# Performance work log

Hardware: AMD Instinct MI355X
Metric: run time of the kernel (lower is better)

The kernel has to match this reference:

```python
import jax, jax.numpy as jnp
import numpy as np

B, T, FB, C = 2, 256, 128, 128
H_T, H_F, BAND = 4, 4, 16
INNER = 4 * C


def setup_inputs() -> dict:
    key = jax.random.key(0)
    ks = jax.random.split(key, 8)
    g = lambda k, shp: jax.random.normal(k, shp, jnp.float32) * 0.02
    return {
        "x": jax.random.normal(ks[0], (B, T, FB, C), jnp.float32),
        # temporal pre-norm + MHA (in_proj [3C,C], out_proj [C,C])
        "ln_t_w": jnp.ones((C,), jnp.float32), "ln_t_b": jnp.zeros((C,), jnp.float32),
        "t_wi": g(ks[1], (3 * C, C)), "t_bi": jnp.zeros((3 * C,), jnp.float32),
        "t_wo": g(ks[2], (C, C)), "t_bo": jnp.zeros((C,), jnp.float32),
        # frequency pre-norm + MHA
        "ln_f_w": jnp.ones((C,), jnp.float32), "ln_f_b": jnp.zeros((C,), jnp.float32),
        "f_wi": g(ks[3], (3 * C, C)), "f_bi": jnp.zeros((3 * C,), jnp.float32),
        "f_wo": g(ks[4], (C, C)), "f_bo": jnp.zeros((C,), jnp.float32),
        # FFN pre-norm + two linears
        "ln_n_w": jnp.ones((C,), jnp.float32), "ln_n_b": jnp.zeros((C,), jnp.float32),
        "w1": g(ks[5], (INNER, C)), "b1": jnp.zeros((INNER,), jnp.float32),
        "w2": g(ks[6], (C, INNER)), "b2": jnp.zeros((C,), jnp.float32),
    }


def _ln(x, w, b, eps=1e-5):
    mu = x.mean(-1, keepdims=True)
    var = ((x - mu) ** 2).mean(-1, keepdims=True)
    return (x - mu) * jax.lax.rsqrt(var + eps) * w + b


def _mha(x, wi, bi, wo, bo, h, mask):
    """torch.nn.MultiheadAttention equivalent. x: [..., S, C], mask: additive [S, S]."""
    c = x.shape[-1]
    dh = c // h
    qkv = x @ wi.T + bi
    q, k, v = jnp.split(qkv, 3, axis=-1)
    split = lambda t: t.reshape(t.shape[:-1] + (h, dh)).swapaxes(-2, -3)  # [..., h, S, dh]
    q, k, v = split(q), split(k), split(v)
    scores = jnp.einsum('...hqd,...hkd->...hqk', q, k) * (1.0 / np.sqrt(dh)) + mask
    attn = jax.nn.softmax(scores, axis=-1)
    o = jnp.einsum('...hqk,...hkd->...hqd', attn, v)
    o = o.swapaxes(-2, -3).reshape(x.shape)
    return o @ wo.T + bo


def _causal_mask(n):
    i = jnp.arange(n)
    return jnp.where(i[:, None] >= i[None, :], 0.0, -jnp.inf).astype(jnp.float32)


def _band_mask(n, band):
    i = jnp.arange(n)
    return jnp.where(jnp.abs(i[:, None] - i[None, :]) <= band, 0.0, -jnp.inf).astype(jnp.float32)


def reference(x, ln_t_w, ln_t_b, t_wi, t_bi, t_wo, t_bo,
              ln_f_w, ln_f_b, f_wi, f_bi, f_wo, f_bo,
              ln_n_w, ln_n_b, w1, b1, w2, b2):
    cm = _causal_mask(x.shape[1])      # [T, T]
    bm = _band_mask(x.shape[2], BAND)  # [F, F]
    # temporal causal MHSA per frequency bin (pre-norm residual)
    xt = _ln(x, ln_t_w, ln_t_b).transpose(0, 2, 1, 3)  # [B, F, T, C]
    x = x + _mha(xt, t_wi, t_bi, t_wo, t_bo, H_T, cm).transpose(0, 2, 1, 3)
    # banded local MHSA over frequency per time step
    xf = _ln(x, ln_f_w, ln_f_b)  # [B, T, F, C]
    x = x + _mha(xf, f_wi, f_bi, f_wo, f_bo, H_F, bm)
    # FFN (Linear -> exact GELU -> Linear)
    xn = _ln(x, ln_n_w, ln_n_b)
    h = jax.nn.gelu(xn @ w1.T + b1, approximate=False)
    x = x + (h @ w2.T + b2)
    return x
```

## Files before the change

kernel.cpp:

```cpp
#include <hip/hip_runtime.h>
#include <math.h>

typedef __bf16 bf16;
typedef __bf16 bf16x8 __attribute__((ext_vector_type(8)));
typedef __bf16 bf16x4 __attribute__((ext_vector_type(4)));
typedef __bf16 bf16x2 __attribute__((ext_vector_type(2)));
typedef float f32x4 __attribute__((ext_vector_type(4)));
typedef float f32x2 __attribute__((ext_vector_type(2)));
typedef float f32x16 __attribute__((ext_vector_type(16)));
typedef unsigned int u32;
typedef unsigned int u32x4 __attribute__((ext_vector_type(4)));

#define AS1 __attribute__((address_space(1)))
#define AS3 __attribute__((address_space(3)))

static __device__ __forceinline__ f32x4 mfma16(bf16x8 a, bf16x8 b, f32x4 c) {
    return __builtin_amdgcn_mfma_f32_16x16x32_bf16(a, b, c, 0, 0, 0);
}
static __device__ __forceinline__ f32x16 mfma32(bf16x8 a, bf16x8 b, f32x16 c) {
    return __builtin_amdgcn_mfma_f32_32x32x16_bf16(a, b, c, 0, 0, 0);
}
static __device__ __forceinline__ u32 pk2(float a, float b) {
    bf16x2 v; v[0] = (bf16)a; v[1] = (bf16)b;
    return __builtin_bit_cast(u32, v);
}
static __device__ __forceinline__ float gelu_f(float x) {
    float u = 0.7978845608f * x * __builtin_fmaf(0.044715f, x * x, 1.0f);
    float e = __expf(2.0f * u);
    return x - x * __builtin_amdgcn_rcpf(e + 1.0f);
}

__global__ __launch_bounds__(256) void cvt_w6(
    const float* __restrict__ s0, const float* __restrict__ s1,
    const float* __restrict__ s2, const float* __restrict__ s3,
    const float* __restrict__ s4, const float* __restrict__ s5,
    bf16* __restrict__ dst)
{
    int i = (blockIdx.x * 256 + threadIdx.x) * 4;
    const float* src; int off;
    if      (i <  49152) { src = s0; off = 0; }
    else if (i <  65536) { src = s1; off = 49152; }
    else if (i < 114688) { src = s2; off = 65536; }
    else if (i < 131072) { src = s3; off = 114688; }
    else if (i < 196608) { src = s4; off = 131072; }
    else                 { src = s5; off = 196608; }
    f32x4 v = *(const f32x4*)&src[i - off];
    bf16x4 b;
    b[0] = (bf16)v[0]; b[1] = (bf16)v[1]; b[2] = (bf16)v[2]; b[3] = (bf16)v[3];
    *(bf16x4*)&dst[i] = b;
}

template<int OUT_BF16, int RES, int RESBF, int GELU_, int LNA, int RMAP, int KT, int NT>
__global__ __launch_bounds__(256) void gemm_rw(
    const bf16* __restrict__ A, const bf16* __restrict__ W,
    const float* __restrict__ bias, const void* __restrict__ res,
    void* __restrict__ outp,
    const float* __restrict__ xf, const float* __restrict__ lnaw,
    const float* __restrict__ lnab)
{
    constexpr int N = NT * 128;
    __shared__ __align__(16) bf16 Bs[128 * 64];
    const int tid  = threadIdx.x;
    const int lane = tid & 63;
    const int w    = tid >> 6;
    const int li = lane & 15, g = lane >> 4;
    const int m0 = blockIdx.x * 64;
    const int arow = m0 + w * 16 + li;
    int srow = arow;
    if constexpr (RMAP) {
        int b = arow >> 15, t = (arow >> 7) & 255, f = arow & 127;
        srow = (b << 15) + (f << 8) + t;
    }
    const bf16* ap = A + (size_t)srow * KT;

    bf16x8 afrag[4];
    if constexpr (LNA) {
        int b = arow >> 15, f = (arow >> 8) & 127, t = arow & 255;
        const float* xp = xf + (((size_t)b * 256 + t) * 128 + f) * 128;
        f32x4 cv[8];
        #pragma unroll
        for (int cc = 0; cc < 4; ++cc) {
            cv[2 * cc]     = *(const f32x4*)&xp[cc * 32 + g * 8];
            cv[2 * cc + 1] = *(const f32x4*)&xp[cc * 32 + g * 8 + 4];
        }
        float sm = 0.f, sq = 0.f;
        #pragma unroll
        for (int i = 0; i < 8; ++i)
            #pragma unroll
            for (int j = 0; j < 4; ++j) { float v = cv[i][j]; sm += v; sq += v * v; }
        sm += __shfl_xor(sm, 16); sm += __shfl_xor(sm, 32);
        sq += __shfl_xor(sq, 16); sq += __shfl_xor(sq, 32);
        float mu = sm * 0.0078125f;
        float rs = rsqrtf(sq * 0.0078125f - mu * mu + 1e-5f);
        #pragma unroll
        for (int cc = 0; cc < 4; ++cc) {
            f32x4 w0 = *(const f32x4*)&lnaw[cc * 32 + g * 8];
            f32x4 w1 = *(const f32x4*)&lnaw[cc * 32 + g * 8 + 4];
            f32x4 b0 = *(const f32x4*)&lnab[cc * 32 + g * 8];
            f32x4 b1 = *(const f32x4*)&lnab[cc * 32 + g * 8 + 4];
            #pragma unroll
            for (int j = 0; j < 4; ++j) {
                afrag[cc][j]     = (bf16)((cv[2 * cc][j]     - mu) * rs * w0[j] + b0[j]);
                afrag[cc][4 + j] = (bf16)((cv[2 * cc + 1][j] - mu) * rs * w1[j] + b1[j]);
            }
        }
    } else if constexpr (KT == 128) {
        #pragma unroll
        for (int cc = 0; cc < 4; ++cc)
            afrag[cc] = *(const bf16x8*)&ap[cc * 32 + g * 8];
    }

    #pragma unroll
    for (int t = 0; t < NT; ++t) {
        const int n0 = t * 128;
        f32x4 acc[8] = {};

        #pragma unroll
        for (int k0 = 0; k0 < KT; k0 += 64) {
            #pragma unroll
            for (int it = 0; it < 4; ++it) {
                int idx = it * 256 + tid;
                int brow = idx >> 3, bch = idx & 7;
                const bf16* gp = W + (size_t)(n0 + brow) * KT + k0 + ((bch ^ (brow & 7)) * 8);
                __builtin_amdgcn_global_load_lds((AS1 void*)gp, (AS3 void*)(Bs + idx * 8), 16, 0, 0);
            }
            bf16x8 av0, av1;
            if constexpr (KT != 128) {
                av0 = *(const bf16x8*)&ap[k0 + g * 8];
                av1 = *(const bf16x8*)&ap[k0 + 32 + g * 8];
            }
            __syncthreads();
            #pragma unroll
            for (int kk = 0; kk < 2; ++kk) {
                bf16x8 av;
                if constexpr (KT == 128) av = afrag[(k0 >> 5) + kk];
                else                     av = kk ? av1 : av0;
                #pragma unroll
                for (int j = 0; j < 8; ++j) {
                    int brow = j * 16 + li;
                    int bch = (kk * 4 + g) ^ (li & 7);
                    bf16x8 bv = *(const bf16x8*)&Bs[brow * 64 + bch * 8];
                    acc[j] = mfma16(av, bv, acc[j]);
                }
            }
            __syncthreads();
        }

        float bcol[8];
        #pragma unroll
        for (int j = 0; j < 8; ++j) bcol[j] = bias[n0 + j * 16 + li];

        const int row0 = m0 + w * 16 + g * 4;
        #pragma unroll
        for (int r = 0; r < 4; ++r) {
            int row = row0 + r;
            #pragma unroll
            for (int j = 0; j < 8; ++j) {
                size_t off = (size_t)row * N + n0 + j * 16 + li;
                float v = acc[j][r] + bcol[j];
                if constexpr (RES) {
                    if constexpr (RESBF) v += (float)((const bf16*)res)[off];
                    else                 v += ((const float*)res)[off];
                }
                if constexpr (GELU_) v = gelu_f(v);
                if constexpr (OUT_BF16) ((bf16*)outp)[off] = (bf16)v;
                else                    ((float*)outp)[off] = v;
            }
        }
    }
}

__global__ __launch_bounds__(256) void ffn_fused(
    const bf16* __restrict__ A, const bf16* __restrict__ W1,
    const float* __restrict__ b1, const bf16* __restrict__ W2,
    const float* __restrict__ b2, const bf16* __restrict__ res,
    float* __restrict__ outp)
{
    __shared__ __align__(16) bf16 Bs[128 * 64];
    __shared__ __align__(16) bf16 hbuf[64 * 136];
    const int tid  = threadIdx.x;
    const int lane = tid & 63;
    const int w    = tid >> 6;
    const int li = lane & 15, g = lane >> 4;
    const int m0 = blockIdx.x * 64;
    const int arow = m0 + w * 16 + li;
    const bf16* ap = A + (size_t)arow * 128;

    bf16x8 axn[4];
    #pragma unroll
    for (int cc = 0; cc < 4; ++cc)
        axn[cc] = *(const bf16x8*)&ap[cc * 32 + g * 8];

    const int sidx_brow = tid >> 1;

    f32x4 oacc[8] = {};

    #pragma unroll
    for (int t = 0; t < 4; ++t) {
        f32x4 hacc[8] = {};
        #pragma unroll
        for (int k0 = 0; k0 < 128; k0 += 64) {
            #pragma unroll
            for (int it = 0; it < 4; ++it) {
                int idx = it * 256 + tid;
                int brow = idx >> 3, bch = idx & 7;
                const bf16* gp = W1 + (size_t)(t * 128 + brow) * 128 + k0 + ((bch ^ (brow & 7)) * 8);
                __builtin_amdgcn_global_load_lds((AS1 void*)gp, (AS3 void*)(Bs + idx * 8), 16, 0, 0);
            }
            __syncthreads();
            #pragma unroll
            for (int kk = 0; kk < 2; ++kk) {
                bf16x8 av = axn[(k0 >> 5) + kk];
                #pragma unroll
                for (int j = 0; j < 8; ++j) {
                    int brow = j * 16 + li;
                    int bch = (kk * 4 + g) ^ (li & 7);
                    bf16x8 bv = *(const bf16x8*)&Bs[brow * 64 + bch * 8];
                    hacc[j] = mfma16(av, bv, hacc[j]);
                }
            }
            __syncthreads();
        }

        #pragma unroll
        for (int it = 0; it < 4; ++it) {
            int idx = it * 256 + tid;
            int brow = idx >> 3, bch = idx & 7;
            const bf16* gp = W2 + (size_t)brow * 512 + t * 128 + ((bch ^ (brow & 7)) * 8);
            __builtin_amdgcn_global_load_lds((AS1 void*)gp, (AS3 void*)(Bs + idx * 8), 16, 0, 0);
        }

        float b1c[8];
        #pragma unroll
        for (int j = 0; j < 8; ++j) b1c[j] = b1[t * 128 + j * 16 + li];
        #pragma unroll
        for (int r = 0; r < 4; ++r) {
            int lrow = w * 16 + g * 4 + r;
            #pragma unroll
            for (int j = 0; j < 8; ++j)
                hbuf[lrow * 136 + j * 16 + li] = (bf16)gelu_f(hacc[j][r] + b1c[j]);
        }
        __syncthreads();

        bf16x8 ah[4];
        #pragma unroll
        for (int cc = 0; cc < 4; ++cc)
            ah[cc] = *(const bf16x8*)&hbuf[(w * 16 + li) * 136 + cc * 32 + g * 8];

        #pragma unroll
        for (int k0 = 0; k0 < 128; k0 += 64) {
            if (k0) {
                #pragma unroll
                for (int it = 0; it < 4; ++it) {
                    int idx = it * 256 + tid;
                    int brow = idx >> 3, bch = idx & 7;
                    const bf16* gp = W2 + (size_t)brow * 512 + t * 128 + k0 + ((bch ^ (brow & 7)) * 8);
                    __builtin_amdgcn_global_load_lds((AS1 void*)gp, (AS3 void*)(Bs + idx * 8), 16, 0, 0);
                }
                __syncthreads();
            }
            #pragma unroll
            for (int kk = 0; kk < 2; ++kk) {
                bf16x8 av = ah[(k0 >> 5) + kk];
                #pragma unroll
                for (int j = 0; j < 8; ++j) {
                    int brow = j * 16 + li;
                    int bch = (kk * 4 + g) ^ (li & 7);
                    bf16x8 bv = *(const bf16x8*)&Bs[brow * 64 + bch * 8];
                    oacc[j] = mfma16(av, bv, oacc[j]);
                }
            }
            __syncthreads();
        }
    }

    float b2c[8];
    #pragma unroll
    for (int j = 0; j < 8; ++j) b2c[j] = b2[j * 16 + li];
    const int row0 = m0 + w * 16 + g * 4;
    #pragma unroll
    for (int r = 0; r < 4; ++r) {
        int row = row0 + r;
        #pragma unroll
        for (int j = 0; j < 8; ++j) {
            size_t off = (size_t)row * 128 + j * 16 + li;
            float v = oacc[j][r] + b2c[j] + (float)res[off];
            outp[off] = v;
        }
    }
}

template<int MODE, int RESBF>
__global__ __launch_bounds__(256) void attn_fused(
    const bf16* __restrict__ qkv, const bf16* __restrict__ Wo,
    const float* __restrict__ bo, const void* __restrict__ res,
    bf16* __restrict__ xc, bf16* __restrict__ xn,
    const float* __restrict__ lnw, const float* __restrict__ lnb)
{
    constexpr int S = (MODE == 0) ? 256 : 128;
    __shared__ __align__(16) char smem[2 * 20480 + 2048];
    float* red = (float*)(smem + 40960);
    const int tid = threadIdx.x;
    const int lane = tid & 63;
    const int w = tid >> 6;
    const int hi = lane >> 5;
    const int q31 = lane & 31;
    const int s = blockIdx.x;
    const int qb = blockIdx.y * 64;

    const size_t base = (size_t)s * S * 384;
    const bf16* qp = qkv + base + w * 32;

    const float sc = 0.17677669529663687f;
    bf16x8 qA0, qA1, qB0, qB1;
    {
        bf16x8 r0 = *(const bf16x8*)&qp[(size_t)(qb + q31) * 384 + hi * 8];
        bf16x8 r1 = *(const bf16x8*)&qp[(size_t)(qb + q31) * 384 + 16 + hi * 8];
        bf16x8 r2 = *(const bf16x8*)&qp[(size_t)(qb + 32 + q31) * 384 + hi * 8];
        bf16x8 r3 = *(const bf16x8*)&qp[(size_t)(qb + 32 + q31) * 384 + 16 + hi * 8];
        #pragma unroll
        for (int e = 0; e < 8; ++e) {
            qA0[e] = (bf16)((float)r0[e] * sc);
            qA1[e] = (bf16)((float)r1[e] * sc);
            qB0[e] = (bf16)((float)r2[e] * sc);
            qB1[e] = (bf16)((float)r3[e] * sc);
        }
    }

    f32x16 OA = {}, OB = {};
    float lA = 0.f, lB = 0.f;

    int klo, khi;
    if constexpr (MODE == 0) { klo = 0; khi = qb + 64; }
    else {
        klo = (qb > 16 ? (qb - 16) : 0) & ~31;
        khi = (qb + 80 < S) ? (qb + 80) : S;
    }

    const int seg = tid & 15, rw = tid >> 4;
    const char* qc = (const char*)qkv + base * 2;
    const int wdst = (seg >> 2) * 2560 + rw * 80 + (seg & 3) * 16;

    u32x4 rk0, rk1, rv0, rv1;
    auto gload = [&](int k0) {
        const char* r0 = qc + (size_t)(k0 + rw) * 768;
        const char* r1 = qc + (size_t)(k0 + rw + 16) * 768;
        rk0 = *(const u32x4*)(r0 + 256 + seg * 16);
        rk1 = *(const u32x4*)(r1 + 256 + seg * 16);
        rv0 = *(const u32x4*)(r0 + 512 + seg * 16);
        rv1 = *(const u32x4*)(r1 + 512 + seg * 16);
    };
    auto swrite = [&](char* buf) {
        *(u32x4*)(buf + wdst)                = rk0;
        *(u32x4*)(buf + wdst + 1280)         = rk1;
        *(u32x4*)(buf + 10240 + wdst)        = rv0;
        *(u32x4*)(buf + 10240 + wdst + 1280) = rv1;
    };

    gload(klo);
    swrite(smem);
    __syncthreads();
    int cur = 0;

    for (int k0 = klo; k0 < khi; k0 += 32) {
        bool notlast = (k0 + 32 < khi);
        if (notlast) gload(k0 + 32);

        char* buf = smem + cur * 20480;
        const char* kb = buf + w * 2560 + q31 * 80 + hi * 16;
        bf16x8 kf0 = *(const bf16x8*)(kb);
        bf16x8 kf1 = *(const bf16x8*)(kb + 32);
        const bf16* vb = (const bf16*)(buf + 10240) + w * 1280 + hi * 320 + q31;
        bf16x8 vf1, vf2;
        #pragma unroll
        for (int e = 0; e < 8; ++e) {
            vf1[e] = vb[e * 40];
            vf2[e] = vb[640 + e * 40];
        }

        auto step = [&](f32x16& O, float& l, bf16x8 q0, bf16x8 q1,
                        int qrow, bool doMask) {
            f32x16 st = {};
            st = mfma32(kf0, q0, st);
            st = mfma32(kf1, q1, st);
            if (doMask) {
                #pragma unroll
                for (int r = 0; r < 16; ++r) {
                    int krow = k0 + (r & 3) + 8 * (r >> 2) + 4 * hi;
                    bool ok;
                    if constexpr (MODE == 0) ok = (krow <= qrow);
                    else { int d = krow - qrow; ok = (d <= 16 && d >= -16); }
                    st[r] = ok ? st[r] : -3.0e38f;
                }
            }
            float ps = 0.f;
            #pragma unroll
            for (int r = 0; r < 16; ++r) {
                float p = __expf(st[r]);
                st[r] = p;
                ps += p;
            }
            ps += __shfl_xor(ps, 32);
            l += ps;

            u32 c01 = pk2(st[0], st[1]),   c23 = pk2(st[2], st[3]);
            u32 c45 = pk2(st[4], st[5]),   c67 = pk2(st[6], st[7]);
            u32 c89 = pk2(st[8], st[9]),   cAB = pk2(st[10], st[11]);
            u32 cCD = pk2(st[12], st[13]), cEF = pk2(st[14], st[15]);
            u32 x01 = __shfl_xor((int)c01, 32), x23 = __shfl_xor((int)c23, 32);
            u32 x45 = __shfl_xor((int)c45, 32), x67 = __shfl_xor((int)c67, 32);
            u32 x89 = __shfl_xor((int)c89, 32), xAB = __shfl_xor((int)cAB, 32);
            u32 xCD = __shfl_xor((int)cCD, 32), xEF = __shfl_xor((int)cEF, 32);
            u32x4 b1w = hi ? u32x4{x45, x67, c45, c67} : u32x4{c01, c23, x01, x23};
            u32x4 b2w = hi ? u32x4{xCD, xEF, cCD, cEF} : u32x4{c89, cAB, x89, xAB};
            bf16x8 B1 = __builtin_bit_cast(bf16x8, b1w);
            bf16x8 B2 = __builtin_bit_cast(bf16x8, b2w);

            O = mfma32(vf1, B1, O);
            O = mfma32(vf2, B2, O);
        };

        bool actA, actB, dgA, dgB;
        if constexpr (MODE == 0) {
            actA = (k0 <= qb); actB = true;
            dgA = (k0 == qb);  dgB = (k0 == qb + 32);
        } else {
            actA = (k0 >= qb - 47) && (k0 <= qb + 47);
            actB = (k0 >= qb - 15) && (k0 <= qb + 79);
            dgA = true; dgB = true;
        }
        if (actA) step(OA, lA, qA0, qA1, qb + q31, dgA);
        if (actB) step(OB, lB, qB0, qB1, qb + 32 + q31, dgB);

        if (notlast) swrite(smem + (cur ^ 1) * 20480);
        __syncthreads();
        cur ^= 1;
    }

    bf16* o_lds = (bf16*)smem;
    float invA = 1.f / lA, invB = 1.f / lB;
    #pragma unroll
    for (int mb = 0; mb < 4; ++mb) {
        bf16x4 ovA, ovB;
        #pragma unroll
        for (int j = 0; j < 4; ++j) {
            ovA[j] = (bf16)(OA[mb * 4 + j] * invA);
            ovB[j] = (bf16)(OB[mb * 4 + j] * invB);
        }
        *(bf16x4*)&o_lds[q31 * 136 + w * 32 + mb * 8 + hi * 4] = ovA;
        *(bf16x4*)&o_lds[(32 + q31) * 136 + w * 32 + mb * 8 + hi * 4] = ovB;
    }
    __syncthreads();

    const int li = lane & 15, g = lane >> 4;
    bf16x8 af[4][4];
    #pragma unroll
    for (int mi = 0; mi < 4; ++mi)
        #pragma unroll
        for (int kk = 0; kk < 4; ++kk)
            af[mi][kk] = *(const bf16x8*)&o_lds[(mi * 16 + li) * 136 + kk * 32 + g * 8];

    f32x4 acc[4][2] = {};
    #pragma unroll
    for (int ni = 0; ni < 2; ++ni) {
        #pragma unroll
        for (int kk = 0; kk < 4; ++kk) {
            bf16x8 bv = *(const bf16x8*)&Wo[(size_t)(w * 32 + ni * 16 + li) * 128 + kk * 32 + g * 8];
            #pragma unroll
            for (int mi = 0; mi < 4; ++mi)
                acc[mi][ni] = mfma16(af[mi][kk], bv, acc[mi][ni]);
        }
    }

    float vals[4][2][4];
    #pragma unroll
    for (int mi = 0; mi < 4; ++mi) {
        #pragma unroll
        for (int r = 0; r < 4; ++r) {
            int lrl = mi * 16 + g * 4 + r;
            int grow = qb + lrl;
            size_t rrow;
            if constexpr (MODE == 0) {
                int b = s >> 7, f = s & 127;
                rrow = ((size_t)(b * 256 + grow)) * 128 + f;
            } else {
                int b = s >> 8, t = s & 255;
                rrow = (size_t)b * 32768 + (size_t)grow * 256 + t;
            }
            #pragma unroll
            for (int ni = 0; ni < 2; ++ni) {
                int col = w * 32 + ni * 16 + li;
                float v = acc[mi][ni][r] + bo[col];
                if constexpr (RESBF) v += (float)((const bf16*)res)[rrow * 128 + col];
                else                 v += ((const float*)res)[rrow * 128 + col];
                vals[mi][ni][r] = v;
            }
        }
    }
    #pragma unroll
    for (int mi = 0; mi < 4; ++mi) {
        #pragma unroll
        for (int r = 0; r < 4; ++r) {
            float sm = vals[mi][0][r] + vals[mi][1][r];
            float sq = vals[mi][0][r] * vals[mi][0][r] + vals[mi][1][r] * vals[mi][1][r];
            #pragma unroll
            for (int off = 1; off < 16; off <<= 1) {
                sm += __shfl_xor(sm, off);
                sq += __shfl_xor(sq, off);
            }
            if (li == 0) {
                red[(mi * 16 + g * 4 + r) * 8 + w * 2 + 0] = sm;
                red[(mi * 16 + g * 4 + r) * 8 + w * 2 + 1] = sq;
            }
        }
    }
    __syncthreads();
    #pragma unroll
    for (int mi = 0; mi < 4; ++mi) {
        #pragma unroll
        for (int r = 0; r < 4; ++r) {
            int mrow = mi * 16 + g * 4 + r;
            f32x4 p0 = *(const f32x4*)&red[mrow * 8 + 0];
            f32x4 p1 = *(const f32x4*)&red[mrow * 8 + 4];
            float smt = p0[0] + p0[2] + p1[0] + p1[2];
            float sqt = p0[1] + p0[3] + p1[1] + p1[3];
            float mu = smt * 0.0078125f;
            float rs = rsqrtf(sqt * 0.0078125f - mu * mu + 1e-5f);
            size_t woff = ((size_t)s * S + qb + mrow) * 128;
            #pragma unroll
            for (int ni = 0; ni < 2; ++ni) {
                int col = w * 32 + ni * 16 + li;
                float v = vals[mi][ni][r];
                xc[woff + col] = (bf16)v;
                xn[woff + col] = (bf16)((v - mu) * rs * lnw[col] + lnb[col]);
            }
        }
    }
}

extern "C" void kernel_launch(void* const* d_in, const int* in_sizes, int n_in,
                              void* d_out, int out_size, void* d_ws, size_t ws_size,
                              hipStream_t stream) {
    const float* x      = (const float*)d_in[0];
    const float* ln_t_w = (const float*)d_in[1];
    const float* ln_t_b = (const float*)d_in[2];
    const float* t_wi   = (const float*)d_in[3];
    const float* t_bi   = (const float*)d_in[4];
    const float* t_wo   = (const float*)d_in[5];
    const float* t_bo   = (const float*)d_in[6];
    const float* ln_f_w = (const float*)d_in[7];
    const float* ln_f_b = (const float*)d_in[8];
    const float* f_wi   = (const float*)d_in[9];
    const float* f_bi   = (const float*)d_in[10];
    const float* f_wo   = (const float*)d_in[11];
    const float* f_bo   = (const float*)d_in[12];
    const float* ln_n_w = (const float*)d_in[13];
    const float* ln_n_b = (const float*)d_in[14];
    const float* w1     = (const float*)d_in[15];
    const float* b1     = (const float*)d_in[16];
    const float* w2     = (const float*)d_in[17];
    const float* b2     = (const float*)d_in[18];

    char* ws = (char*)d_ws;
    bf16* wbf  = (bf16*)ws;
    bf16* xn   = (bf16*)(ws + 524288);
    bf16* qkvh = (bf16*)(ws + 524288 + 16777216);
    bf16* xcA  = (bf16*)(ws + 524288 + 16777216 + 67108864 + 16777216);
    bf16* xcB  = (bf16*)(ws + 524288 + 16777216 + 67108864 + 2 * 16777216);
    float* out = (float*)d_out;

    const bf16* twi_b = wbf + 0;
    const bf16* two_b = wbf + 49152;
    const bf16* fwi_b = wbf + 65536;
    const bf16* fwo_b = wbf + 114688;
    const bf16* w1_b  = wbf + 131072;
    const bf16* w2_b  = wbf + 196608;

    cvt_w6<<<256, 256, 0, stream>>>(t_wi, t_wo, f_wi, f_wo, w1, w2, wbf);

    gemm_rw<1, 0, 0, 0, 1, 0, 128, 3><<<1024, 256, 0, stream>>>(
        nullptr, twi_b, t_bi, nullptr, qkvh, x, ln_t_w, ln_t_b);
    attn_fused<0, 0><<<dim3(256, 4), 256, 0, stream>>>(
        qkvh, two_b, t_bo, x, xcA, xn, ln_f_w, ln_f_b);

    gemm_rw<1, 0, 0, 0, 0, 1, 128, 3><<<1024, 256, 0, stream>>>(
        xn, fwi_b, f_bi, nullptr, qkvh, nullptr, nullptr, nullptr);
    attn_fused<1, 1><<<dim3(512, 2), 256, 0, stream>>>(
        qkvh, fwo_b, f_bo, xcA, xcB, xn, ln_n_w, ln_n_b);

    ffn_fused<<<1024, 256, 0, stream>>>(xn, w1_b, b1, w2_b, b2, xcB, out);

    (void)in_sizes; (void)n_in; (void)out_size; (void)ws_size;
}
```

Before: 154.2 us.

## Double-buffer weight tiles in fused FFN kernel to overlap loads with MFMA

The FFN kernel's single shared weight tile becomes two ping-pong buffers. The next W1 or W2 64-column chunk is issued with global_load_lds while the MFMAs run on the current chunk, which hides global-to-LDS latency behind compute. The barrier between the GELU write to hbuf and the read back is dropped, since each wave only reads the rows it wrote itself. This costs an extra 16 KB of LDS per block, which may reduce occupancy.

```diff
diff --git a/kernel.cpp b/kernel.cpp
--- a/kernel.cpp
+++ b/kernel.cpp
@@ -176,7 +176,7 @@
     const float* __restrict__ b2, const bf16* __restrict__ res,
     float* __restrict__ outp)
 {
-    __shared__ __align__(16) bf16 Bs[128 * 64];
+    __shared__ __align__(16) bf16 Bs[2][128 * 64];
     __shared__ __align__(16) bf16 hbuf[64 * 136];
     const int tid  = threadIdx.x;
     const int lane = tid & 63;
@@ -191,44 +191,53 @@
     for (int cc = 0; cc < 4; ++cc)
         axn[cc] = *(const bf16x8*)&ap[cc * 32 + g * 8];
 
-    const int sidx_brow = tid >> 1;
+    const int sidx  = tid;
+    auto stageW1 = [&](int b, int t, int k0) {
+        #pragma unroll
+        for (int it = 0; it < 4; ++it) {
+            int idx = it * 256 + sidx;
+            int brow = idx >> 3, bch = idx & 7;
+            const bf16* gp = W1 + (size_t)(t * 128 + brow) * 128 + k0 + ((bch ^ (brow & 7)) * 8);
+            __builtin_amdgcn_global_load_lds((AS1 void*)gp, (AS3 void*)(Bs[b] + idx * 8), 16, 0, 0);
+        }
+    };
+    auto stageW2 = [&](int b, int t, int k0) {
+        #pragma unroll
+        for (int it = 0; it < 4; ++it) {
+            int idx = it * 256 + sidx;
+            int brow = idx >> 3, bch = idx & 7;
+            const bf16* gp = W2 + (size_t)brow * 512 + t * 128 + k0 + ((bch ^ (brow & 7)) * 8);
+            __builtin_amdgcn_global_load_lds((AS1 void*)gp, (AS3 void*)(Bs[b] + idx * 8), 16, 0, 0);
+        }
+    };
+    auto compute16 = [&](int b, bf16x8 av0, bf16x8 av1, f32x4* acc) {
+        #pragma unroll
+        for (int kk = 0; kk < 2; ++kk) {
+            bf16x8 av = kk ? av1 : av0;
+            #pragma unroll
+            for (int j = 0; j < 8; ++j) {
+                int brow = j * 16 + li;
+                int bch = (kk * 4 + g) ^ (li & 7);
+                bf16x8 bv = *(const bf16x8*)&Bs[b][brow * 64 + bch * 8];
+                acc[j] = mfma16(av, bv, acc[j]);
+            }
+        }
+    };
 
     f32x4 oacc[8] = {};
 
+    stageW1(0, 0, 0);
     #pragma unroll
     for (int t = 0; t < 4; ++t) {
         f32x4 hacc[8] = {};
-        #pragma unroll
-        for (int k0 = 0; k0 < 128; k0 += 64) {
-            #pragma unroll
-            for (int it = 0; it < 4; ++it) {
-                int idx = it * 256 + tid;
-                int brow = idx >> 3, bch = idx & 7;
-                const bf16* gp = W1 + (size_t)(t * 128 + brow) * 128 + k0 + ((bch ^ (brow & 7)) * 8);
-                __builtin_amdgcn_global_load_lds((AS1 void*)gp, (AS3 void*)(Bs + idx * 8), 16, 0, 0);
-            }
-            __syncthreads();
-            #pragma unroll
-            for (int kk = 0; kk < 2; ++kk) {
-                bf16x8 av = axn[(k0 >> 5) + kk];
-                #pragma unroll
-                for (int j = 0; j < 8; ++j) {
-                    int brow = j * 16 + li;
-                    int bch = (kk * 4 + g) ^ (li & 7);
-                    bf16x8 bv = *(const bf16x8*)&Bs[brow * 64 + bch * 8];
-                    hacc[j] = mfma16(av, bv, hacc[j]);
-                }
-            }
-            __syncthreads();
-        }
-
-        #pragma unroll
-        for (int it = 0; it < 4; ++it) {
-            int idx = it * 256 + tid;
-            int brow = idx >> 3, bch = idx & 7;
-            const bf16* gp = W2 + (size_t)brow * 512 + t * 128 + ((bch ^ (brow & 7)) * 8);
-            __builtin_amdgcn_global_load_lds((AS1 void*)gp, (AS3 void*)(Bs + idx * 8), 16, 0, 0);
-        }
+
+        __syncthreads();
+        stageW1(1, t, 64);
+        compute16(0, axn[0], axn[1], hacc);
+
+        __syncthreads();
+        stageW2(0, t, 0);
+        compute16(1, axn[2], axn[3], hacc);
 
         float b1c[8];
         #pragma unroll
@@ -240,38 +249,18 @@
             for (int j = 0; j < 8; ++j)
                 hbuf[lrow * 136 + j * 16 + li] = (bf16)gelu_f(hacc[j][r] + b1c[j]);
         }
-        __syncthreads();
-
         bf16x8 ah[4];
         #pragma unroll
         for (int cc = 0; cc < 4; ++cc)
             ah[cc] = *(const bf16x8*)&hbuf[(w * 16 + li) * 136 + cc * 32 + g * 8];
 
-        #pragma unroll
-        for (int k0 = 0; k0 < 128; k0 += 64) {
-            if (k0) {
-                #pragma unroll
-                for (int it = 0; it < 4; ++it) {
-                    int idx = it * 256 + tid;
-                    int brow = idx >> 3, bch = idx & 7;
-                    const bf16* gp = W2 + (size_t)brow * 512 + t * 128 + k0 + ((bch ^ (brow & 7)) * 8);
-                    __builtin_amdgcn_global_load_lds((AS1 void*)gp, (AS3 void*)(Bs + idx * 8), 16, 0, 0);
-                }
-                __syncthreads();
-            }
-            #pragma unroll
-            for (int kk = 0; kk < 2; ++kk) {
-                bf16x8 av = ah[(k0 >> 5) + kk];
-                #pragma unroll
-                for (int j = 0; j < 8; ++j) {
-                    int brow = j * 16 + li;
-                    int bch = (kk * 4 + g) ^ (li & 7);
-                    bf16x8 bv = *(const bf16x8*)&Bs[brow * 64 + bch * 8];
-                    oacc[j] = mfma16(av, bv, oacc[j]);
-                }
-            }
-            __syncthreads();
-        }
+        __syncthreads();
+        stageW2(1, t, 64);
+        compute16(0, ah[0], ah[1], oacc);
+
+        __syncthreads();
+        if (t < 3) stageW1(0, t + 1, 0);
+        compute16(1, ah[2], ah[3], oacc);
     }
 
     float b2c[8];
@@ -284,8 +273,7 @@
         #pragma unroll
         for (int j = 0; j < 8; ++j) {
             size_t off = (size_t)row * 128 + j * 16 + li;
-            float v = oacc[j][r] + b2c[j] + (float)res[off];
-            outp[off] = v;
+            outp[off] = oacc[j][r] + b2c[j] + (float)res[off];
         }
     }
 }
```

New measurement: 158.4 us. 2.7% more time.
